# Kernel tuning notes

Hardware: AMD Instinct MI355X
Metric: run time of the kernel (lower is better)

Reference implementation:

```python
import jax, jax.numpy as jnp
import numpy as np
from jax.scipy.special import logsumexp

EPSILON = 0.01      # Sinkhorn entropic regularization
MAX_ITERATIONS = 50 # Sinkhorn iterations (init kwarg)
NEG_INF = -1e9      # finite stand-in for log(0) to keep grads clean


def setup_inputs() -> dict:
    key = jax.random.key(0)
    k1, k2, k3 = jax.random.split(key, 3)
    B, S, P, D = 8, 2048, 1024, 2
    predictions = jax.random.normal(k1, (B, S, D), dtype=jnp.float32)
    positions = jax.random.normal(k2, (B, P, D), dtype=jnp.float32)
    labels = jax.random.randint(k3, (B, S), 0, P)
    return {"predictions": predictions, "labels": labels, "positions": positions}


def _sinkhorn_loss(predictions, positions, labels):
    B, S, D = predictions.shape
    P = positions.shape[1]
    dt = predictions.dtype

    # target weights = normalized label histogram over the P positions
    w = jnp.zeros((B, P), dt).at[jnp.arange(B)[:, None], labels].add(1.0) / S
    log_a = jnp.full((B, S), -jnp.log(jnp.asarray(S, dt)), dtype=dt)  # uniform source
    log_b = jnp.where(w > 0, jnp.log(jnp.maximum(w, 1e-30)), NEG_INF)

    # squared-Euclidean cost matrix [B, S, P]
    x2 = jnp.sum(predictions * predictions, axis=-1)  # [B,S]
    y2 = jnp.sum(positions * positions, axis=-1)      # [B,P]
    xy = jnp.einsum('bsd,bpd->bsp', predictions, positions)
    C = jnp.maximum(x2[:, :, None] + y2[:, None, :] - 2.0 * xy, 0.0)
    mK = -C / EPSILON  # log-kernel

    def step(carry, _):
        f, g = carry
        f = EPSILON * (log_a - logsumexp(mK + g[:, None, :] / EPSILON, axis=2))
        g = EPSILON * (log_b - logsumexp(mK + f[:, :, None] / EPSILON, axis=1))
        return (f, g), None

    f0 = jnp.zeros((B, S), dt)
    g0 = jnp.zeros((B, P), dt)
    (f, g), _ = jax.lax.scan(step, (f0, g0), None, length=MAX_ITERATIONS)

    # transport plan in log domain; distance = <P, C>
    logT = mK + f[:, :, None] / EPSILON + g[:, None, :] / EPSILON
    dist = jnp.sum(jnp.exp(logT) * C, axis=(1, 2))  # [B]
    return jnp.mean(dist)  # reduction='mean'


def reference(predictions, labels, positions):
    return _sinkhorn_loss(predictions, positions, labels)
```

## Files before the change

kernel.cpp:

```cpp
#include <hip/hip_runtime.h>
#include <math.h>


#define BB 8
#define SS 2048
#define PP 1024
#define NEG_INF -1e9f
#define LOG2S 11.0f
#define ITERS 50
#define K2E 144.269504088896f
#define TWOK 288.539008177792f
#define NBLK 256
#define NTHR 1024

typedef float v2f __attribute__((ext_vector_type(2)));

__device__ __forceinline__ float fexp2(float x) {
  return __builtin_amdgcn_exp2f(x);
}
__device__ __forceinline__ float flog2(float x) {
  return __builtin_amdgcn_logf(x);
}
__device__ __forceinline__ v2f vfma(v2f a, v2f b, v2f c) {
  return __builtin_elementwise_fma(a, b, c);
}
__device__ __forceinline__ v2f vmax(v2f a, v2f b) {
  return __builtin_elementwise_max(a, b);
}

__device__ __forceinline__ float coh_load(const float* p) {
  return __hip_atomic_load((float*)p, __ATOMIC_RELAXED, __HIP_MEMORY_SCOPE_AGENT);
}
__device__ __forceinline__ void coh_store(float* p, float v) {
  __hip_atomic_store(p, v, __ATOMIC_RELAXED, __HIP_MEMORY_SCOPE_AGENT);
}
__device__ __forceinline__ int coh_loadi(const int* p) {
  return __hip_atomic_load((int*)p, __ATOMIC_RELAXED, __HIP_MEMORY_SCOPE_AGENT);
}
__device__ __forceinline__ void coh_storei(int* p, int v) {
  __hip_atomic_store(p, v, __ATOMIC_RELAXED, __HIP_MEMORY_SCOPE_AGENT);
}

__device__ __forceinline__ void batch_barrier(int* slots, int sub, int phase,
                                              int w, int lane) {
  __syncthreads();
  asm volatile("" ::: "memory");
  if (threadIdx.x == 0) coh_storei(&slots[sub], phase);
  if (w == 0) {
    for (;;) {
      int v = (lane < 32) ? coh_loadi(&slots[lane]) : 0x7fffffff;
      if (__all(v >= phase)) break;
      __builtin_amdgcn_s_sleep(1);
    }
  }
  asm volatile("" ::: "memory");
  __syncthreads();
}


__global__ __launch_bounds__(1024) void setup_kernel(
    const int* __restrict__ labels, float* __restrict__ G2,
    float* __restrict__ logb2, int* __restrict__ slots,
    float* __restrict__ out) {
  __shared__ int c[PP];
  int b = blockIdx.x;
  int t = threadIdx.x;
  c[t] = 0;
  __syncthreads();
  atomicAdd(&c[labels[b * SS + t] & (PP - 1)], 1);
  atomicAdd(&c[labels[b * SS + PP + t] & (PP - 1)], 1);
  __syncthreads();
  int cc = c[t];
  logb2[b * PP + t] = (cc > 0) ? (flog2((float)cc) - LOG2S) : NEG_INF;
  G2[b * PP + t] = 0.0f;
  if (t < 32) slots[(b << 5) + t] = 0;
  if (t == 0 && b == 0) out[0] = 0.0f;
}

__global__ __launch_bounds__(1024) void sinkhorn_persist(
    const float* __restrict__ preds, const float* __restrict__ pos,
    const float* __restrict__ logb2, float* __restrict__ F2g,
    float* __restrict__ G2g, int* __restrict__ slots,
    float* __restrict__ out) {
  __shared__ __align__(16) float fy0[PP], fy1[PP], fq[PP];
  __shared__ __align__(16) float gx0[SS], gx1[SS], gq[SS];
  __shared__ float spart;
  const int t = threadIdx.x;
  const int blk = blockIdx.x;
  const int bb = blk >> 5;
  const int sub = blk & 31;
  int* myslots = slots + (bb << 5);
  const float2* pos2 = (const float2*)pos;
  const float2* preds2 = (const float2*)preds;
  float* G2b = G2g + (bb << 10);
  float* F2b = F2g + (bb << 11);

  float yr2, xr2[2];
  {
    float2 y = pos2[(bb << 10) + t];
    yr2 = y.x * y.x + y.y * y.y;
    fy0[t] = y.x;
    fy1[t] = y.y;
  }
#pragma unroll
  for (int k = 0; k < 2; ++k) {
    int e = t + (k << 10);
    float2 x = preds2[(bb << 11) + e];
    xr2[k] = x.x * x.x + x.y * x.y;
    gx0[e] = x.x;
    gx1[e] = x.y;
  }

  const int w = t >> 6, lane = t & 63;
  const int frowb = (blk << 6) + (w << 2);
  float fk0[4], fk1[4], fc0[4];
#pragma unroll
  for (int r = 0; r < 4; ++r) {
    float2 fx = preds2[frowb + r];
    fk0[r] = TWOK * fx.x;
    fk1[r] = TWOK * fx.y;
    fc0[r] = fmaf(K2E, fx.x * fx.x + fx.y * fx.y, -LOG2S);
  }
  const int gcolb = (blk << 5) + (w << 1);
  float gk0[2], gk1[2], gc0[2];
#pragma unroll
  for (int c = 0; c < 2; ++c) {
    float2 gy = pos2[gcolb + c];
    gk0[c] = TWOK * gy.x;
    gk1[c] = TWOK * gy.y;
    gc0[c] = fmaf(K2E, gy.x * gy.x + gy.y * gy.y, logb2[gcolb + c]);
  }

  for (int it = 0; it < ITERS; ++it) {
    fq[t] = fmaf(-K2E, yr2, coh_load(&G2b[t]));
    __syncthreads();
    {
      float m[4];
      v2f s[4];
#pragma unroll
      for (int r = 0; r < 4; ++r) { m[r] = -3.4e38f; s[r] = (v2f)(0.0f); }
#pragma unroll
      for (int ch = 0; ch < 2; ++ch) {
        v2f a0[4], a1[4], aq[4];
#pragma unroll
        for (int i = 0; i < 4; ++i) {
          int pi = (ch << 8) + (i << 6) + lane;
          a0[i] = *(const v2f*)&fy0[pi << 1];
          a1[i] = *(const v2f*)&fy1[pi << 1];
          aq[i] = *(const v2f*)&fq[pi << 1];
        }
#pragma unroll
        for (int r = 0; r < 4; ++r) {
          v2f K0 = (v2f)(fk0[r]), K1 = (v2f)(fk1[r]);
          v2f u0 = vfma(K0, a0[0], vfma(K1, a1[0], aq[0]));
          v2f u1 = vfma(K0, a0[1], vfma(K1, a1[1], aq[1]));
          v2f u2 = vfma(K0, a0[2], vfma(K1, a1[2], aq[2]));
          v2f u3 = vfma(K0, a0[3], vfma(K1, a1[3], aq[3]));
          v2f cm2 = vmax(vmax(u0, u1), vmax(u2, u3));
          float mn = fmaxf(m[r], fmaxf(cm2.x, cm2.y));
          float sc = fexp2(m[r] - mn);
          v2f mn2 = (v2f)(mn);
          v2f d0 = u0 - mn2, d1 = u1 - mn2, d2 = u2 - mn2, d3 = u3 - mn2;
          v2f e0 = {fexp2(d0.x), fexp2(d0.y)};
          v2f e1 = {fexp2(d1.x), fexp2(d1.y)};
          v2f e2 = {fexp2(d2.x), fexp2(d2.y)};
          v2f e3 = {fexp2(d3.x), fexp2(d3.y)};
          s[r] = vfma(s[r], (v2f)(sc), (e0 + e1) + (e2 + e3));
          m[r] = mn;
        }
      }
      float fout = 0.0f;
#pragma unroll
      for (int r = 0; r < 4; ++r) {
        float M = m[r];
#pragma unroll
        for (int off = 1; off <= 32; off <<= 1)
          M = fmaxf(M, __shfl_xor(M, off, 64));
        float sr = (s[r].x + s[r].y) * fexp2(m[r] - M);
#pragma unroll
        for (int off = 1; off <= 32; off <<= 1) sr += __shfl_xor(sr, off, 64);
        float v = fc0[r] - M - flog2(sr);
        if (lane == r) fout = v;
      }
      if (lane < 4) coh_store(&F2g[frowb + lane], fout);
    }
    batch_barrier(myslots, sub, 2 * it + 1, w, lane);

#pragma unroll
    for (int k = 0; k < 2; ++k) {
      int e = t + (k << 10);
      gq[e] = fmaf(-K2E, xr2[k], coh_load(&F2b[e]));
    }
    __syncthreads();
    {
      float m[2];
      v2f s[2];
#pragma unroll
      for (int c = 0; c < 2; ++c) { m[c] = -3.4e38f; s[c] = (v2f)(0.0f); }
#pragma unroll
      for (int ch = 0; ch < 4; ++ch) {
        v2f a0[4], a1[4], aq[4];
#pragma unroll
        for (int i = 0; i < 4; ++i) {
          int pi = (ch << 8) + (i << 6) + lane;
          a0[i] = *(const v2f*)&gx0[pi << 1];
          a1[i] = *(const v2f*)&gx1[pi << 1];
          aq[i] = *(const v2f*)&gq[pi << 1];
        }
#pragma unroll
        for (int c = 0; c < 2; ++c) {
          v2f K0 = (v2f)(gk0[c]), K1 = (v2f)(gk1[c]);
          v2f u0 = vfma(K0, a0[0], vfma(K1, a1[0], aq[0]));
          v2f u1 = vfma(K0, a0[1], vfma(K1, a1[1], aq[1]));
          v2f u2 = vfma(K0, a0[2], vfma(K1, a1[2], aq[2]));
          v2f u3 = vfma(K0, a0[3], vfma(K1, a1[3], aq[3]));
          v2f cm2 = vmax(vmax(u0, u1), vmax(u2, u3));
          float mn = fmaxf(m[c], fmaxf(cm2.x, cm2.y));
          float sc = fexp2(m[c] - mn);
          v2f mn2 = (v2f)(mn);
          v2f d0 = u0 - mn2, d1 = u1 - mn2, d2 = u2 - mn2, d3 = u3 - mn2;
          v2f e0 = {fexp2(d0.x), fexp2(d0.y)};
          v2f e1 = {fexp2(d1.x), fexp2(d1.y)};
          v2f e2 = {fexp2(d2.x), fexp2(d2.y)};
          v2f e3 = {fexp2(d3.x), fexp2(d3.y)};
          s[c] = vfma(s[c], (v2f)(sc), (e0 + e1) + (e2 + e3));
          m[c] = mn;
        }
      }
      float gout = 0.0f;
#pragma unroll
      for (int c = 0; c < 2; ++c) {
        float M = m[c];
#pragma unroll
        for (int off = 1; off <= 32; off <<= 1)
          M = fmaxf(M, __shfl_xor(M, off, 64));
        float sr = (s[c].x + s[c].y) * fexp2(m[c] - M);
#pragma unroll
        for (int off = 1; off <= 32; off <<= 1) sr += __shfl_xor(sr, off, 64);
        float v = gc0[c] - M - flog2(sr);
        if (lane == c) gout = v;
      }
      if (lane < 2) coh_store(&G2g[gcolb + lane], gout);
    }
    batch_barrier(myslots, sub, 2 * it + 2, w, lane);
  }

  if (t == 0) spart = 0.0f;
  fq[t] = fmaf(-K2E, yr2, coh_load(&G2b[t]));
  __syncthreads();
  float acc = 0.0f;
#pragma unroll
  for (int rr = 0; rr < 4; ++rr) {
    int row = frowb + rr;
    float2 x = preds2[row];
    float x2 = x.x * x.x + x.y * x.y;
    float qx = fmaf(-K2E, x2, coh_load(&F2g[row]));
#pragma unroll
    for (int i = 0; i < 16; ++i) {
      int p = (i << 6) + lane;
      float ay0 = fy0[p], ay1 = fy1[p], aqz = fq[p];
      float y2 = fmaf(ay0, ay0, ay1 * ay1);
      float tt = fmaf(x.y, ay1, x.x * ay0);
      float c = fmaxf(x2 + y2 - 2.0f * tt, 0.0f);
      float v2 = fmaf(TWOK, tt, aqz + qx);
      acc = fmaf(fexp2(v2), c, acc);
    }
  }
#pragma unroll
  for (int off = 32; off; off >>= 1) acc += __shfl_xor(acc, off, 64);
  if (lane == 0) atomicAdd(&spart, acc);
  __syncthreads();
  if (t == 0) atomicAdd(out, spart * (1.0f / (float)BB));
}

extern "C" void kernel_launch(void* const* d_in, const int* in_sizes, int n_in,
                              void* d_out, int out_size, void* d_ws,
                              size_t ws_size, hipStream_t stream) {
  const float* preds = (const float*)d_in[0];
  const int* labels = (const int*)d_in[1];
  const float* pos = (const float*)d_in[2];
  float* out = (float*)d_out;
  char* ws = (char*)d_ws;
  float* G2 = (float*)(ws);
  float* F2 = (float*)(ws + 32768);
  float* logb2 = (float*)(ws + 98304);
  int* slots = (int*)(ws + 131072);

  hipLaunchKernelGGL(setup_kernel, dim3(BB), dim3(1024), 0, stream, labels, G2,
                     logb2, slots, out);
  hipLaunchKernelGGL(sinkhorn_persist, dim3(NBLK), dim3(NTHR), 0, stream,
                     preds, pos, logb2, F2, G2, slots, out);
}
```

Measured before the change: 567.0 us.

## Interleave two batches per block with split arrive/wait barriers

Each block now serves two batches, A and B, with 64 blocks per batch pair instead of 32 blocks per batch. The fused barrier is split into separate arrive and wait steps with per-phase done counters, so the f/g phase for one batch can run while the other batch's blocks are still arriving. This is meant to hide the cross-block barrier latency. The g phase also splits each column's logsumexp across 4 waves and merges partials in shared memory, and it reads x coordinates straight from global memory as float4. In exchange it adds more barriers per iteration, more LDS use, and extra global loads.

```diff
diff --git a/kernel.cpp b/kernel.cpp
--- a/kernel.cpp
+++ b/kernel.cpp
@@ -41,15 +41,16 @@
   __hip_atomic_store(p, v, __ATOMIC_RELAXED, __HIP_MEMORY_SCOPE_AGENT);
 }
 
-__device__ __forceinline__ void batch_barrier(int* slots, int sub, int phase,
-                                              int w, int lane) {
+__device__ __forceinline__ void arrive(int* slot, int ver) {
   __syncthreads();
   asm volatile("" ::: "memory");
-  if (threadIdx.x == 0) coh_storei(&slots[sub], phase);
+  if (threadIdx.x == 0) coh_storei(slot, ver);
+}
+__device__ __forceinline__ void wait_all(int* slots, int ver, int w, int lane) {
   if (w == 0) {
     for (;;) {
-      int v = (lane < 32) ? coh_loadi(&slots[lane]) : 0x7fffffff;
-      if (__all(v >= phase)) break;
+      int v = coh_loadi(&slots[lane]);
+      if (__all(v >= ver)) break;
       __builtin_amdgcn_s_sleep(1);
     }
   }
@@ -60,8 +61,8 @@
 
 __global__ __launch_bounds__(1024) void setup_kernel(
     const int* __restrict__ labels, float* __restrict__ G2,
-    float* __restrict__ logb2, int* __restrict__ slots,
-    float* __restrict__ out) {
+    float* __restrict__ logb2, int* __restrict__ fdone,
+    int* __restrict__ gdone, float* __restrict__ out) {
   __shared__ int c[PP];
   int b = blockIdx.x;
   int t = threadIdx.x;
@@ -73,192 +74,256 @@
   int cc = c[t];
   logb2[b * PP + t] = (cc > 0) ? (flog2((float)cc) - LOG2S) : NEG_INF;
   G2[b * PP + t] = 0.0f;
-  if (t < 32) slots[(b << 5) + t] = 0;
+  if (t < 64) {
+    fdone[(b << 6) + t] = 0;
+    gdone[(b << 6) + t] = 0;
+  }
   if (t == 0 && b == 0) out[0] = 0.0f;
+}
+
+__device__ __forceinline__ void f_phase(const float* fy0, const float* fy1,
+                                        const float* fq,
+                                        const float2* preds2, int frow,
+                                        float* F2out, int lane) {
+  float2 fx0 = preds2[frow];
+  float2 fx1 = preds2[frow + 1];
+  float fk0[2] = {TWOK * fx0.x, TWOK * fx1.x};
+  float fk1[2] = {TWOK * fx0.y, TWOK * fx1.y};
+  float fc0[2] = {fmaf(K2E, fx0.x * fx0.x + fx0.y * fx0.y, -LOG2S),
+                  fmaf(K2E, fx1.x * fx1.x + fx1.y * fx1.y, -LOG2S)};
+  float m[2];
+  v2f s[2];
+#pragma unroll
+  for (int r = 0; r < 2; ++r) { m[r] = -3.4e38f; s[r] = (v2f)(0.0f); }
+#pragma unroll
+  for (int ch = 0; ch < 2; ++ch) {
+    v2f a0[4], a1[4], aq[4];
+#pragma unroll
+    for (int i = 0; i < 4; ++i) {
+      int pi = (ch << 8) + (i << 6) + lane;
+      a0[i] = *(const v2f*)&fy0[pi << 1];
+      a1[i] = *(const v2f*)&fy1[pi << 1];
+      aq[i] = *(const v2f*)&fq[pi << 1];
+    }
+#pragma unroll
+    for (int r = 0; r < 2; ++r) {
+      v2f K0 = (v2f)(fk0[r]), K1 = (v2f)(fk1[r]);
+      v2f u0 = vfma(K0, a0[0], vfma(K1, a1[0], aq[0]));
+      v2f u1 = vfma(K0, a0[1], vfma(K1, a1[1], aq[1]));
+      v2f u2 = vfma(K0, a0[2], vfma(K1, a1[2], aq[2]));
+      v2f u3 = vfma(K0, a0[3], vfma(K1, a1[3], aq[3]));
+      v2f cm2 = vmax(vmax(u0, u1), vmax(u2, u3));
+      float mn = fmaxf(m[r], fmaxf(cm2.x, cm2.y));
+      float sc = fexp2(m[r] - mn);
+      v2f mn2 = (v2f)(mn);
+      v2f d0 = u0 - mn2, d1 = u1 - mn2, d2 = u2 - mn2, d3 = u3 - mn2;
+      v2f e0 = {fexp2(d0.x), fexp2(d0.y)};
+      v2f e1 = {fexp2(d1.x), fexp2(d1.y)};
+      v2f e2 = {fexp2(d2.x), fexp2(d2.y)};
+      v2f e3 = {fexp2(d3.x), fexp2(d3.y)};
+      s[r] = vfma(s[r], (v2f)(sc), (e0 + e1) + (e2 + e3));
+      m[r] = mn;
+    }
+  }
+  float fout = 0.0f;
+#pragma unroll
+  for (int r = 0; r < 2; ++r) {
+    float M = m[r];
+#pragma unroll
+    for (int off = 1; off <= 32; off <<= 1)
+      M = fmaxf(M, __shfl_xor(M, off, 64));
+    float sr = (s[r].x + s[r].y) * fexp2(m[r] - M);
+#pragma unroll
+    for (int off = 1; off <= 32; off <<= 1) sr += __shfl_xor(sr, off, 64);
+    float v = fc0[r] - M - flog2(sr);
+    if (lane == r) fout = v;
+  }
+  if (lane < 2) coh_store(&F2out[lane], fout);
+}
+
+__device__ __forceinline__ void g_phase(const float4* x4, const float* gq,
+                                        const float2* pos2,
+                                        const float* __restrict__ logb2,
+                                        int gcol, int w, int tq, int lane,
+                                        float2 (*part)[4], float* G2out) {
+  float gk0[4], gk1[4], gc0[4];
+#pragma unroll
+  for (int c = 0; c < 4; ++c) {
+    float2 gy = pos2[gcol + c];
+    gk0[c] = TWOK * gy.x;
+    gk1[c] = TWOK * gy.y;
+    gc0[c] = fmaf(K2E, gy.x * gy.x + gy.y * gy.y, logb2[gcol + c]);
+  }
+  v2f a0[4], a1[4], aq[4];
+#pragma unroll
+  for (int i = 0; i < 4; ++i) {
+    int pi = (tq << 8) + (i << 6) + lane;
+    float4 v = x4[pi];
+    a0[i] = (v2f){v.x, v.z};
+    a1[i] = (v2f){v.y, v.w};
+    aq[i] = *(const v2f*)&gq[pi << 1];
+  }
+  float2 myp = make_float2(0.0f, 0.0f);
+#pragma unroll
+  for (int c = 0; c < 4; ++c) {
+    v2f K0 = (v2f)(gk0[c]), K1 = (v2f)(gk1[c]);
+    v2f u0 = vfma(K0, a0[0], vfma(K1, a1[0], aq[0]));
+    v2f u1 = vfma(K0, a0[1], vfma(K1, a1[1], aq[1]));
+    v2f u2 = vfma(K0, a0[2], vfma(K1, a1[2], aq[2]));
+    v2f u3 = vfma(K0, a0[3], vfma(K1, a1[3], aq[3]));
+    v2f cm2 = vmax(vmax(u0, u1), vmax(u2, u3));
+    float M = fmaxf(cm2.x, cm2.y);
+#pragma unroll
+    for (int off = 1; off <= 32; off <<= 1)
+      M = fmaxf(M, __shfl_xor(M, off, 64));
+    v2f M2 = (v2f)(M);
+    v2f d0 = u0 - M2, d1 = u1 - M2, d2 = u2 - M2, d3 = u3 - M2;
+    v2f es = ((v2f){fexp2(d0.x), fexp2(d0.y)} +
+              (v2f){fexp2(d1.x), fexp2(d1.y)}) +
+             ((v2f){fexp2(d2.x), fexp2(d2.y)} +
+              (v2f){fexp2(d3.x), fexp2(d3.y)});
+    float S = es.x + es.y;
+#pragma unroll
+    for (int off = 1; off <= 32; off <<= 1) S += __shfl_xor(S, off, 64);
+    if (lane == c) myp = make_float2(M - gc0[c], S);
+  }
+  if (lane < 4) part[w][lane] = myp;
+  __syncthreads();
+  if (tq == 0 && lane < 4) {
+    float2 p0 = part[w][lane], p1 = part[w + 1][lane];
+    float2 p2 = part[w + 2][lane], p3 = part[w + 3][lane];
+    float M = fmaxf(fmaxf(p0.x, p1.x), fmaxf(p2.x, p3.x));
+    float S = p0.y * fexp2(p0.x - M) + p1.y * fexp2(p1.x - M) +
+              p2.y * fexp2(p2.x - M) + p3.y * fexp2(p3.x - M);
+    coh_store(&G2out[lane], -M - flog2(S));
+  }
 }
 
 __global__ __launch_bounds__(1024) void sinkhorn_persist(
     const float* __restrict__ preds, const float* __restrict__ pos,
     const float* __restrict__ logb2, float* __restrict__ F2g,
-    float* __restrict__ G2g, int* __restrict__ slots,
-    float* __restrict__ out) {
-  __shared__ __align__(16) float fy0[PP], fy1[PP], fq[PP];
-  __shared__ __align__(16) float gx0[SS], gx1[SS], gq[SS];
+    float* __restrict__ G2g, int* __restrict__ fdone,
+    int* __restrict__ gdone, float* __restrict__ out) {
+  __shared__ __align__(16) float fy0A[PP], fy1A[PP], fqA[PP];
+  __shared__ __align__(16) float fy0B[PP], fy1B[PP], fqB[PP];
+  __shared__ __align__(16) float gqA[SS], gqB[SS];
+  __shared__ float2 part[16][4];
   __shared__ float spart;
   const int t = threadIdx.x;
   const int blk = blockIdx.x;
-  const int bb = blk >> 5;
-  const int sub = blk & 31;
-  int* myslots = slots + (bb << 5);
+  const int grp = blk >> 6;
+  const int sub = blk & 63;
+  const int bbA = grp << 1, bbB = (grp << 1) + 1;
+  int* fdA = fdone + (bbA << 6);
+  int* fdB = fdone + (bbB << 6);
+  int* gdA = gdone + (bbA << 6);
+  int* gdB = gdone + (bbB << 6);
   const float2* pos2 = (const float2*)pos;
   const float2* preds2 = (const float2*)preds;
-  float* G2b = G2g + (bb << 10);
-  float* F2b = F2g + (bb << 11);
-
-  float yr2, xr2[2];
+  const float4* xA4 = (const float4*)(preds + ((size_t)bbA << 12));
+  const float4* xB4 = (const float4*)(preds + ((size_t)bbB << 12));
+  float* G2A = G2g + (bbA << 10);
+  float* G2B = G2g + (bbB << 10);
+  float* F2A = F2g + (bbA << 11);
+  float* F2B = F2g + (bbB << 11);
+
+  float yr2A, yr2B, xr2A[2], xr2B[2];
   {
-    float2 y = pos2[(bb << 10) + t];
-    yr2 = y.x * y.x + y.y * y.y;
-    fy0[t] = y.x;
-    fy1[t] = y.y;
+    float2 y = pos2[(bbA << 10) + t];
+    yr2A = y.x * y.x + y.y * y.y;
+    fy0A[t] = y.x;
+    fy1A[t] = y.y;
+  }
+  {
+    float2 y = pos2[(bbB << 10) + t];
+    yr2B = y.x * y.x + y.y * y.y;
+    fy0B[t] = y.x;
+    fy1B[t] = y.y;
   }
 #pragma unroll
   for (int k = 0; k < 2; ++k) {
     int e = t + (k << 10);
-    float2 x = preds2[(bb << 11) + e];
-    xr2[k] = x.x * x.x + x.y * x.y;
-    gx0[e] = x.x;
-    gx1[e] = x.y;
+    float2 xa = preds2[(bbA << 11) + e];
+    xr2A[k] = xa.x * xa.x + xa.y * xa.y;
+    float2 xb = preds2[(bbB << 11) + e];
+    xr2B[k] = xb.x * xb.x + xb.y * xb.y;
   }
 
   const int w = t >> 6, lane = t & 63;
-  const int frowb = (blk << 6) + (w << 2);
-  float fk0[4], fk1[4], fc0[4];
-#pragma unroll
-  for (int r = 0; r < 4; ++r) {
-    float2 fx = preds2[frowb + r];
-    fk0[r] = TWOK * fx.x;
-    fk1[r] = TWOK * fx.y;
-    fc0[r] = fmaf(K2E, fx.x * fx.x + fx.y * fx.y, -LOG2S);
-  }
-  const int gcolb = (blk << 5) + (w << 1);
-  float gk0[2], gk1[2], gc0[2];
-#pragma unroll
-  for (int c = 0; c < 2; ++c) {
-    float2 gy = pos2[gcolb + c];
-    gk0[c] = TWOK * gy.x;
-    gk1[c] = TWOK * gy.y;
-    gc0[c] = fmaf(K2E, gy.x * gy.x + gy.y * gy.y, logb2[gcolb + c]);
-  }
+  const int frowA = (bbA << 11) + (sub << 5) + (w << 1);
+  const int frowB = (bbB << 11) + (sub << 5) + (w << 1);
+  const int cg = w >> 2, tq = w & 3;
+  const int gcolA = (bbA << 10) + (sub << 4) + (cg << 2);
+  const int gcolB = (bbB << 10) + (sub << 4) + (cg << 2);
 
   for (int it = 0; it < ITERS; ++it) {
-    fq[t] = fmaf(-K2E, yr2, coh_load(&G2b[t]));
+    wait_all(gdA, it, w, lane);
+    fqA[t] = fmaf(-K2E, yr2A, coh_load(&G2A[t]));
     __syncthreads();
-    {
-      float m[4];
-      v2f s[4];
-#pragma unroll
-      for (int r = 0; r < 4; ++r) { m[r] = -3.4e38f; s[r] = (v2f)(0.0f); }
-#pragma unroll
-      for (int ch = 0; ch < 2; ++ch) {
-        v2f a0[4], a1[4], aq[4];
-#pragma unroll
-        for (int i = 0; i < 4; ++i) {
-          int pi = (ch << 8) + (i << 6) + lane;
-          a0[i] = *(const v2f*)&fy0[pi << 1];
-          a1[i] = *(const v2f*)&fy1[pi << 1];
-          aq[i] = *(const v2f*)&fq[pi << 1];
-        }
-#pragma unroll
-        for (int r = 0; r < 4; ++r) {
-          v2f K0 = (v2f)(fk0[r]), K1 = (v2f)(fk1[r]);
-          v2f u0 = vfma(K0, a0[0], vfma(K1, a1[0], aq[0]));
-          v2f u1 = vfma(K0, a0[1], vfma(K1, a1[1], aq[1]));
-          v2f u2 = vfma(K0, a0[2], vfma(K1, a1[2], aq[2]));
-          v2f u3 = vfma(K0, a0[3], vfma(K1, a1[3], aq[3]));
-          v2f cm2 = vmax(vmax(u0, u1), vmax(u2, u3));
-          float mn = fmaxf(m[r], fmaxf(cm2.x, cm2.y));
-          float sc = fexp2(m[r] - mn);
-          v2f mn2 = (v2f)(mn);
-          v2f d0 = u0 - mn2, d1 = u1 - mn2, d2 = u2 - mn2, d3 = u3 - mn2;
-          v2f e0 = {fexp2(d0.x), fexp2(d0.y)};
-          v2f e1 = {fexp2(d1.x), fexp2(d1.y)};
-          v2f e2 = {fexp2(d2.x), fexp2(d2.y)};
-          v2f e3 = {fexp2(d3.x), fexp2(d3.y)};
-          s[r] = vfma(s[r], (v2f)(sc), (e0 + e1) + (e2 + e3));
-          m[r] = mn;
-        }
-      }
-      float fout = 0.0f;
-#pragma unroll
-      for (int r = 0; r < 4; ++r) {
-        float M = m[r];
-#pragma unroll
-        for (int off = 1; off <= 32; off <<= 1)
-          M = fmaxf(M, __shfl_xor(M, off, 64));
-        float sr = (s[r].x + s[r].y) * fexp2(m[r] - M);
-#pragma unroll
-        for (int off = 1; off <= 32; off <<= 1) sr += __shfl_xor(sr, off, 64);
-        float v = fc0[r] - M - flog2(sr);
-        if (lane == r) fout = v;
-      }
-      if (lane < 4) coh_store(&F2g[frowb + lane], fout);
-    }
-    batch_barrier(myslots, sub, 2 * it + 1, w, lane);
-
+    f_phase(fy0A, fy1A, fqA, preds2, frowA, F2g + frowA, lane);
+    arrive(&fdA[sub], it + 1);
+
+    wait_all(gdB, it, w, lane);
+    fqB[t] = fmaf(-K2E, yr2B, coh_load(&G2B[t]));
+    __syncthreads();
+    f_phase(fy0B, fy1B, fqB, preds2, frowB, F2g + frowB, lane);
+    arrive(&fdB[sub], it + 1);
+
+    wait_all(fdA, it + 1, w, lane);
 #pragma unroll
     for (int k = 0; k < 2; ++k) {
       int e = t + (k << 10);
-      gq[e] = fmaf(-K2E, xr2[k], coh_load(&F2b[e]));
+      gqA[e] = fmaf(-K2E, xr2A[k], coh_load(&F2A[e]));
     }
     __syncthreads();
-    {
-      float m[2];
-      v2f s[2];
-#pragma unroll
-      for (int c = 0; c < 2; ++c) { m[c] = -3.4e38f; s[c] = (v2f)(0.0f); }
-#pragma unroll
-      for (int ch = 0; ch < 4; ++ch) {
-        v2f a0[4], a1[4], aq[4];
-#pragma unroll
-        for (int i = 0; i < 4; ++i) {
-          int pi = (ch << 8) + (i << 6) + lane;
-          a0[i] = *(const v2f*)&gx0[pi << 1];
-          a1[i] = *(const v2f*)&gx1[pi << 1];
-          aq[i] = *(const v2f*)&gq[pi << 1];
-        }
-#pragma unroll
-        for (int c = 0; c < 2; ++c) {
-          v2f K0 = (v2f)(gk0[c]), K1 = (v2f)(gk1[c]);
-          v2f u0 = vfma(K0, a0[0], vfma(K1, a1[0], aq[0]));
-          v2f u1 = vfma(K0, a0[1], vfma(K1, a1[1], aq[1]));
-          v2f u2 = vfma(K0, a0[2], vfma(K1, a1[2], aq[2]));
-          v2f u3 = vfma(K0, a0[3], vfma(K1, a1[3], aq[3]));
-          v2f cm2 = vmax(vmax(u0, u1), vmax(u2, u3));
-          float mn = fmaxf(m[c], fmaxf(cm2.x, cm2.y));
-          float sc = fexp2(m[c] - mn);
-          v2f mn2 = (v2f)(mn);
-          v2f d0 = u0 - mn2, d1 = u1 - mn2, d2 = u2 - mn2, d3 = u3 - mn2;
-          v2f e0 = {fexp2(d0.x), fexp2(d0.y)};
-          v2f e1 = {fexp2(d1.x), fexp2(d1.y)};
-          v2f e2 = {fexp2(d2.x), fexp2(d2.y)};
-          v2f e3 = {fexp2(d3.x), fexp2(d3.y)};
-          s[c] = vfma(s[c], (v2f)(sc), (e0 + e1) + (e2 + e3));
-          m[c] = mn;
-        }
-      }
-      float gout = 0.0f;
-#pragma unroll
-      for (int c = 0; c < 2; ++c) {
-        float M = m[c];
-#pragma unroll
-        for (int off = 1; off <= 32; off <<= 1)
-          M = fmaxf(M, __shfl_xor(M, off, 64));
-        float sr = (s[c].x + s[c].y) * fexp2(m[c] - M);
-#pragma unroll
-        for (int off = 1; off <= 32; off <<= 1) sr += __shfl_xor(sr, off, 64);
-        float v = gc0[c] - M - flog2(sr);
-        if (lane == c) gout = v;
-      }
-      if (lane < 2) coh_store(&G2g[gcolb + lane], gout);
-    }
-    batch_barrier(myslots, sub, 2 * it + 2, w, lane);
-  }
-
+    g_phase(xA4, gqA, pos2, logb2, gcolA, w, tq, lane, part, G2g + gcolA);
+    arrive(&gdA[sub], it + 1);
+
+    wait_all(fdB, it + 1, w, lane);
+#pragma unroll
+    for (int k = 0; k < 2; ++k) {
+      int e = t + (k << 10);
+      gqB[e] = fmaf(-K2E, xr2B[k], coh_load(&F2B[e]));
+    }
+    __syncthreads();
+    g_phase(xB4, gqB, pos2, logb2, gcolB, w, tq, lane, part, G2g + gcolB);
+    arrive(&gdB[sub], it + 1);
+  }
+
+  wait_all(gdA, ITERS, w, lane);
+  wait_all(gdB, ITERS, w, lane);
   if (t == 0) spart = 0.0f;
-  fq[t] = fmaf(-K2E, yr2, coh_load(&G2b[t]));
+  fqA[t] = fmaf(-K2E, yr2A, coh_load(&G2A[t]));
+  fqB[t] = fmaf(-K2E, yr2B, coh_load(&G2B[t]));
   __syncthreads();
   float acc = 0.0f;
 #pragma unroll
-  for (int rr = 0; rr < 4; ++rr) {
-    int row = frowb + rr;
+  for (int rr = 0; rr < 2; ++rr) {
+    int row = frowA + rr;
     float2 x = preds2[row];
     float x2 = x.x * x.x + x.y * x.y;
     float qx = fmaf(-K2E, x2, coh_load(&F2g[row]));
 #pragma unroll
     for (int i = 0; i < 16; ++i) {
       int p = (i << 6) + lane;
-      float ay0 = fy0[p], ay1 = fy1[p], aqz = fq[p];
+      float ay0 = fy0A[p], ay1 = fy1A[p], aqz = fqA[p];
+      float y2 = fmaf(ay0, ay0, ay1 * ay1);
+      float tt = fmaf(x.y, ay1, x.x * ay0);
+      float c = fmaxf(x2 + y2 - 2.0f * tt, 0.0f);
+      float v2 = fmaf(TWOK, tt, aqz + qx);
+      acc = fmaf(fexp2(v2), c, acc);
+    }
+  }
+#pragma unroll
+  for (int rr = 0; rr < 2; ++rr) {
+    int row = frowB + rr;
+    float2 x = preds2[row];
+    float x2 = x.x * x.x + x.y * x.y;
+    float qx = fmaf(-K2E, x2, coh_load(&F2g[row]));
+#pragma unroll
+    for (int i = 0; i < 16; ++i) {
+      int p = (i << 6) + lane;
+      float ay0 = fy0B[p], ay1 = fy1B[p], aqz = fqB[p];
       float y2 = fmaf(ay0, ay0, ay1 * ay1);
       float tt = fmaf(x.y, ay1, x.x * ay0);
       float c = fmaxf(x2 + y2 - 2.0f * tt, 0.0f);
@@ -284,10 +349,11 @@
   float* G2 = (float*)(ws);
   float* F2 = (float*)(ws + 32768);
   float* logb2 = (float*)(ws + 98304);
-  int* slots = (int*)(ws + 131072);
+  int* fdone = (int*)(ws + 131072);
+  int* gdone = (int*)(ws + 133120);
 
   hipLaunchKernelGGL(setup_kernel, dim3(BB), dim3(1024), 0, stream, labels, G2,
-                     logb2, slots, out);
+                     logb2, fdone, gdone, out);
   hipLaunchKernelGGL(sinkhorn_persist, dim3(NBLK), dim3(NTHR), 0, stream,
-                     preds, pos, logb2, F2, G2, slots, out);
-}
+                     preds, pos, logb2, F2, G2, fdone, gdone, out);
+}
```

Result: slower. 777.0 us (+37.0%).

## Replace per-batch spin barriers with stamped value flags for dataflow sync

Applied to the files above, without the earlier changes.

Each F and G potential is now stored as a 64-bit word packing the float value with an iteration stamp. Consumers spin on the individual values they need instead of waiting at a 32-block batch barrier after each half-step. This removes two global barriers and their extra __syncthreads per iteration, so blocks can proceed as soon as their inputs are ready. In exchange, every thread polls global memory with 64-bit atomic loads, which doubles the size of the exchanged data and may add memory traffic from polling.

```diff
diff --git a/kernel.cpp b/kernel.cpp
--- a/kernel.cpp
+++ b/kernel.cpp
@@ -14,6 +14,7 @@
 #define NTHR 1024
 
 typedef float v2f __attribute__((ext_vector_type(2)));
+typedef unsigned long long u64;
 
 __device__ __forceinline__ float fexp2(float x) {
   return __builtin_amdgcn_exp2f(x);
@@ -28,40 +29,28 @@
   return __builtin_elementwise_max(a, b);
 }
 
-__device__ __forceinline__ float coh_load(const float* p) {
-  return __hip_atomic_load((float*)p, __ATOMIC_RELAXED, __HIP_MEMORY_SCOPE_AGENT);
-}
-__device__ __forceinline__ void coh_store(float* p, float v) {
+__device__ __forceinline__ u64 coh_load64(const u64* p) {
+  return __hip_atomic_load((u64*)p, __ATOMIC_RELAXED, __HIP_MEMORY_SCOPE_AGENT);
+}
+__device__ __forceinline__ void coh_store64(u64* p, u64 v) {
   __hip_atomic_store(p, v, __ATOMIC_RELAXED, __HIP_MEMORY_SCOPE_AGENT);
 }
-__device__ __forceinline__ int coh_loadi(const int* p) {
-  return __hip_atomic_load((int*)p, __ATOMIC_RELAXED, __HIP_MEMORY_SCOPE_AGENT);
-}
-__device__ __forceinline__ void coh_storei(int* p, int v) {
-  __hip_atomic_store(p, v, __ATOMIC_RELAXED, __HIP_MEMORY_SCOPE_AGENT);
-}
-
-__device__ __forceinline__ void batch_barrier(int* slots, int sub, int phase,
-                                              int w, int lane) {
-  __syncthreads();
-  asm volatile("" ::: "memory");
-  if (threadIdx.x == 0) coh_storei(&slots[sub], phase);
-  if (w == 0) {
-    for (;;) {
-      int v = (lane < 32) ? coh_loadi(&slots[lane]) : 0x7fffffff;
-      if (__all(v >= phase)) break;
-      __builtin_amdgcn_s_sleep(1);
-    }
-  }
-  asm volatile("" ::: "memory");
-  __syncthreads();
+__device__ __forceinline__ u64 pack_vs(float val, unsigned stamp) {
+  return ((u64)stamp << 32) | (u64)__float_as_uint(val);
+}
+__device__ __forceinline__ float wait_val(const u64* p, unsigned stamp) {
+  u64 v = coh_load64(p);
+  while ((unsigned)(v >> 32) != stamp) {
+    __builtin_amdgcn_s_sleep(1);
+    v = coh_load64(p);
+  }
+  return __uint_as_float((unsigned)v);
 }
 
 
 __global__ __launch_bounds__(1024) void setup_kernel(
-    const int* __restrict__ labels, float* __restrict__ G2,
-    float* __restrict__ logb2, int* __restrict__ slots,
-    float* __restrict__ out) {
+    const int* __restrict__ labels, u64* __restrict__ G2v,
+    float* __restrict__ logb2, float* __restrict__ out) {
   __shared__ int c[PP];
   int b = blockIdx.x;
   int t = threadIdx.x;
@@ -72,28 +61,24 @@
   __syncthreads();
   int cc = c[t];
   logb2[b * PP + t] = (cc > 0) ? (flog2((float)cc) - LOG2S) : NEG_INF;
-  G2[b * PP + t] = 0.0f;
-  if (t < 32) slots[(b << 5) + t] = 0;
+  G2v[b * PP + t] = pack_vs(0.0f, 0u);
   if (t == 0 && b == 0) out[0] = 0.0f;
 }
 
 __global__ __launch_bounds__(1024) void sinkhorn_persist(
     const float* __restrict__ preds, const float* __restrict__ pos,
-    const float* __restrict__ logb2, float* __restrict__ F2g,
-    float* __restrict__ G2g, int* __restrict__ slots,
-    float* __restrict__ out) {
+    const float* __restrict__ logb2, u64* __restrict__ F2v,
+    u64* __restrict__ G2v, float* __restrict__ out) {
   __shared__ __align__(16) float fy0[PP], fy1[PP], fq[PP];
   __shared__ __align__(16) float gx0[SS], gx1[SS], gq[SS];
   __shared__ float spart;
   const int t = threadIdx.x;
   const int blk = blockIdx.x;
   const int bb = blk >> 5;
-  const int sub = blk & 31;
-  int* myslots = slots + (bb << 5);
+  u64* G2b = G2v + (bb << 10);
+  u64* F2b = F2v + (bb << 11);
   const float2* pos2 = (const float2*)pos;
   const float2* preds2 = (const float2*)preds;
-  float* G2b = G2g + (bb << 10);
-  float* F2b = F2g + (bb << 11);
 
   float yr2, xr2[2];
   {
@@ -132,7 +117,9 @@
   }
 
   for (int it = 0; it < ITERS; ++it) {
-    fq[t] = fmaf(-K2E, yr2, coh_load(&G2b[t]));
+    const unsigned sF = (unsigned)(it + 1);
+    const unsigned sG = (unsigned)it;
+    fq[t] = fmaf(-K2E, yr2, wait_val(&G2b[t], sG));
     __syncthreads();
     {
       float m[4];
@@ -182,14 +169,13 @@
         float v = fc0[r] - M - flog2(sr);
         if (lane == r) fout = v;
       }
-      if (lane < 4) coh_store(&F2g[frowb + lane], fout);
-    }
-    batch_barrier(myslots, sub, 2 * it + 1, w, lane);
+      if (lane < 4) coh_store64(&F2v[frowb + lane], pack_vs(fout, sF));
+    }
 
 #pragma unroll
     for (int k = 0; k < 2; ++k) {
       int e = t + (k << 10);
-      gq[e] = fmaf(-K2E, xr2[k], coh_load(&F2b[e]));
+      gq[e] = fmaf(-K2E, xr2[k], wait_val(&F2b[e], sF));
     }
     __syncthreads();
     {
@@ -240,13 +226,12 @@
         float v = gc0[c] - M - flog2(sr);
         if (lane == c) gout = v;
       }
-      if (lane < 2) coh_store(&G2g[gcolb + lane], gout);
-    }
-    batch_barrier(myslots, sub, 2 * it + 2, w, lane);
+      if (lane < 2) coh_store64(&G2v[gcolb + lane], pack_vs(gout, sF));
+    }
   }
 
   if (t == 0) spart = 0.0f;
-  fq[t] = fmaf(-K2E, yr2, coh_load(&G2b[t]));
+  fq[t] = fmaf(-K2E, yr2, wait_val(&G2b[t], (unsigned)ITERS));
   __syncthreads();
   float acc = 0.0f;
 #pragma unroll
@@ -254,7 +239,7 @@
     int row = frowb + rr;
     float2 x = preds2[row];
     float x2 = x.x * x.x + x.y * x.y;
-    float qx = fmaf(-K2E, x2, coh_load(&F2g[row]));
+    float qx = fmaf(-K2E, x2, wait_val(&F2v[row], (unsigned)ITERS));
 #pragma unroll
     for (int i = 0; i < 16; ++i) {
       int p = (i << 6) + lane;
@@ -281,13 +266,12 @@
   const float* pos = (const float*)d_in[2];
   float* out = (float*)d_out;
   char* ws = (char*)d_ws;
-  float* G2 = (float*)(ws);
-  float* F2 = (float*)(ws + 32768);
-  float* logb2 = (float*)(ws + 98304);
-  int* slots = (int*)(ws + 131072);
-
-  hipLaunchKernelGGL(setup_kernel, dim3(BB), dim3(1024), 0, stream, labels, G2,
-                     logb2, slots, out);
+  u64* G2v = (u64*)(ws);
+  u64* F2v = (u64*)(ws + 65536);
+  float* logb2 = (float*)(ws + 196608);
+
+  hipLaunchKernelGGL(setup_kernel, dim3(BB), dim3(1024), 0, stream, labels,
+                     G2v, logb2, out);
   hipLaunchKernelGGL(sinkhorn_persist, dim3(NBLK), dim3(NTHR), 0, stream,
-                     preds, pos, logb2, F2, G2, slots, out);
-}
+                     preds, pos, logb2, F2v, G2v, out);
+}
```

Result: slower. 612.0 us (+7.9%).
